# Kernel optimization log

Measured on AMD Instinct MI355X. Metric: run time of the kernel, lower is better.

The kernel has to match this reference:

```python
import jax, jax.numpy as jnp
import numpy as np

N_NODES = 50000
N_EDGES = 800000


def _gcn_conv(x, W, b, src, dst, norm, n_nodes):
    # PyG GCNConv: out = D^{-1/2} (A + I) D^{-1/2} (x W) + b
    h = x @ W                                  # [N, out]
    msg = h[src] * norm[:, None]               # [E+N, out] gathered, normalized messages
    agg = jax.ops.segment_sum(msg, dst, num_segments=n_nodes)
    return agg + b


def _build_norm(edge_index, n_nodes):
    # add self-loops, compute symmetric degree normalization
    loop = jnp.arange(n_nodes, dtype=edge_index.dtype)
    src = jnp.concatenate([edge_index[0], loop])
    dst = jnp.concatenate([edge_index[1], loop])
    deg = jnp.zeros((n_nodes,), jnp.float32).at[dst].add(1.0)
    dinv = jnp.where(deg > 0, jax.lax.rsqrt(deg), 0.0)
    norm = dinv[src] * dinv[dst]
    return src, dst, norm


def setup_inputs() -> dict:
    key = jax.random.key(0)
    ks = jax.random.split(key, 5)
    x = jax.random.normal(ks[0], (N_NODES, 128), dtype=jnp.float32)
    edge_index = jax.random.randint(ks[1], (2, N_EDGES), 0, N_NODES, dtype=jnp.int64)
    s1 = 1.0 / np.sqrt(128)
    s2 = 1.0 / np.sqrt(128)
    s3 = 1.0 / np.sqrt(64)
    return {
        "x": x,
        "edge_index": edge_index,
        "W1": jax.random.normal(ks[2], (128, 128), dtype=jnp.float32) * s1,
        "b1": jnp.zeros((128,), jnp.float32),
        "W2": jax.random.normal(ks[3], (128, 64), dtype=jnp.float32) * s2,
        "b2": jnp.zeros((64,), jnp.float32),
        "W3": jax.random.normal(ks[4], (64, 128), dtype=jnp.float32) * s3,
        "b3": jnp.zeros((128,), jnp.float32),
    }


def reference(x, edge_index, W1, b1, W2, b2, W3, b3):
    n = x.shape[0]
    src, dst, norm = _build_norm(edge_index, n)
    # dropout is identity in eval mode
    h = jax.nn.relu(_gcn_conv(x, W1, b1, src, dst, norm, n))
    h = jax.nn.relu(_gcn_conv(h, W2, b2, src, dst, norm, n))
    out = _gcn_conv(h, W3, b3, src, dst, norm, n)
    return out
```

## Files before the change

kernel.cpp:

```cpp
#include <hip/hip_runtime.h>


#define DEV_INLINE __device__ __forceinline__

typedef unsigned int uint;
typedef unsigned short ushort;
typedef __attribute__((ext_vector_type(8))) short bf16x8;
typedef __attribute__((ext_vector_type(4))) float f32x4;

static DEV_INLINE uint f2bf_rne(float f) {
    uint u = __float_as_uint(f);
    return (u + 0x7FFFu + ((u >> 16) & 1u)) >> 16;
}
static DEV_INLINE uint pack2(float a, float b) { return f2bf_rne(a) | (f2bf_rne(b) << 16); }
static DEV_INLINE float bflo(uint u) { return __uint_as_float(u << 16); }
static DEV_INLINE float bfhi(uint u) { return __uint_as_float(u & 0xFFFF0000u); }

static DEV_INLINE void fma8(float4& a, float4& b, float n, const uint4& v) {
    a.x = fmaf(n, bflo(v.x), a.x); a.y = fmaf(n, bfhi(v.x), a.y);
    a.z = fmaf(n, bflo(v.y), a.z); a.w = fmaf(n, bfhi(v.y), a.w);
    b.x = fmaf(n, bflo(v.z), b.x); b.y = fmaf(n, bfhi(v.z), b.y);
    b.z = fmaf(n, bflo(v.w), b.z); b.w = fmaf(n, bfhi(v.w), b.w);
}

static DEV_INLINE void split8(const float4& x0, const float4& x1, bf16x8& ah, bf16x8& al) {
    float xs[8] = {x0.x, x0.y, x0.z, x0.w, x1.x, x1.y, x1.z, x1.w};
#pragma unroll
    for (int j = 0; j < 8; ++j) {
        uint u = __float_as_uint(xs[j]);
        ah[j] = (short)(u >> 16);
        float r = xs[j] - __uint_as_float(u & 0xFFFF0000u);
        al[j] = (short)(__float_as_uint(r) >> 16);
    }
}


__global__ __launch_bounds__(256) void hist_coarse_kernel(
    const int* __restrict__ dst, int* __restrict__ cnt196, int E, int NBK)
{
    __shared__ int h[256];
    if ((int)threadIdx.x < NBK) h[threadIdx.x] = 0;
    __syncthreads();
    for (int i = blockIdx.x * blockDim.x + threadIdx.x; i < E; i += gridDim.x * blockDim.x)
        atomicAdd(&h[dst[i] >> 8], 1);
    __syncthreads();
    if ((int)threadIdx.x < NBK) {
        int v = h[threadIdx.x];
        if (v) atomicAdd(&cnt196[threadIdx.x], v);
    }
}

__global__ void scan_coarse_kernel(const int* __restrict__ cnt196, int* __restrict__ base196,
                                   int* __restrict__ cursor196, int* __restrict__ rowptr,
                                   int NBK, int N, int E)
{
    __shared__ int buf[256];
    const int tid = threadIdx.x;
    int v = (tid < NBK) ? cnt196[tid] : 0;
    buf[tid] = v;
    __syncthreads();
#pragma unroll
    for (int ofs = 1; ofs < 256; ofs <<= 1) {
        int t = (tid >= ofs) ? buf[tid - ofs] : 0;
        __syncthreads();
        buf[tid] += t;
        __syncthreads();
    }
    if (tid < NBK) {
        int b = buf[tid] - v;
        base196[tid] = b;
        cursor196[tid] = b;
    }
    if (tid == 0) rowptr[N] = E;
}

__global__ __launch_bounds__(256) void scatter_coarse_kernel(
    const int* __restrict__ src, const int* __restrict__ dst,
    int* __restrict__ cursor196, uint* __restrict__ pkg, int E, int NBK)
{
    __shared__ int histL[256];
    __shared__ int baseL[256];
    const int tid = threadIdx.x;
    const int c0  = blockIdx.x * 2048;
    if (tid < NBK) histL[tid] = 0;
    __syncthreads();

    uint mypk[8];
    int  myn = 0;
#pragma unroll
    for (int k = 0; k < 8; ++k) {
        int idx = c0 + k * 256 + tid;
        if (idx < E) {
            uint pk = ((uint)dst[idx] << 16) | (uint)(src[idx] & 0xFFFF);
            mypk[myn++] = pk;
            atomicAdd(&histL[pk >> 24], 1);
        }
    }
    __syncthreads();
    if (tid < NBK) {
        int h = histL[tid];
        baseL[tid] = (h > 0) ? atomicAdd(&cursor196[tid], h) : 0;
        histL[tid] = 0;
    }
    __syncthreads();
    for (int k = 0; k < myn; ++k) {
        uint pk = mypk[k];
        int b = pk >> 24;
        int pos = baseL[b] + atomicAdd(&histL[b], 1);
        pkg[pos] = pk;
    }
}

__global__ __launch_bounds__(256) void build_fine_kernel(
    const uint* __restrict__ pkg, const int* __restrict__ cnt196,
    const int* __restrict__ base196, int* __restrict__ rowptr,
    float* __restrict__ dinv, ushort* __restrict__ perm, int N)
{
    __shared__ uint   pkL[8192];
    __shared__ ushort outS[8192];
    __shared__ int hist[256];
    __shared__ int buf[256];
    const int b   = blockIdx.x;
    const int tid = threadIdx.x;
    const int base = base196[b];
    int nE = cnt196[b];
    if (nE > 8192) nE = 8192;

    hist[tid] = 0;
    __syncthreads();
    for (int i = tid; i < nE; i += 256) {
        uint pk = pkg[base + i];
        pkL[i] = pk;
        atomicAdd(&hist[(pk >> 16) & 255], 1);
    }
    __syncthreads();

    int cnt = hist[tid];
    buf[tid] = cnt;
    __syncthreads();
#pragma unroll
    for (int ofs = 1; ofs < 256; ofs <<= 1) {
        int t = (tid >= ofs) ? buf[tid - ofs] : 0;
        __syncthreads();
        buf[tid] += t;
        __syncthreads();
    }
    int excl = buf[tid] - cnt;
    int node = b * 256 + tid;
    if (node < N) {
        rowptr[node] = base + excl;
        dinv[node]   = rsqrtf((float)(cnt + 1));
    }
    hist[tid] = excl;
    __syncthreads();
    for (int i = tid; i < nE; i += 256) {
        uint pk = pkL[i];
        int d = (pk >> 16) & 255;
        int pos = atomicAdd(&hist[d], 1);
        outS[pos] = (ushort)(pk & 0xFFFFu);
    }
    __syncthreads();
    for (int i = tid; i < nE; i += 256) perm[base + i] = outS[i];
}


template<int K, int NOUT>
static DEV_INLINE void prep_one(const float* __restrict__ W,
                                ushort* __restrict__ Wh, ushort* __restrict__ Wl, int id) {
    constexpr int C = NOUT / 16;
    int lane = id & 63;
    int tc   = id >> 6;
    int c = tc % C, t = tc / C;
    int krow = t * 32 + (lane >> 4) * 8;
    int col  = c * 16 + (lane & 15);
#pragma unroll
    for (int j = 0; j < 8; ++j) {
        float w = W[(size_t)(krow + j) * NOUT + col];
        uint u = __float_as_uint(w);
        Wh[(size_t)id * 8 + j] = (ushort)(u >> 16);
        float r = w - __uint_as_float(u & 0xFFFF0000u);
        Wl[(size_t)id * 8 + j] = (ushort)(__float_as_uint(r) >> 16);
    }
}

__global__ void prep_wfrag_all_kernel(
    const float* __restrict__ W1, const float* __restrict__ W2, const float* __restrict__ W3,
    ushort* w1h, ushort* w1l, ushort* w2h, ushort* w2l, ushort* w3h, ushort* w3l)
{
    int id = blockIdx.x * 256 + threadIdx.x;
    if (id < 2048)       prep_one<128, 128>(W1, w1h, w1l, id);
    else if (id < 3072)  prep_one<128, 64>(W2, w2h, w2l, id - 2048);
    else if (id < 4096)  prep_one<64, 128>(W3, w3h, w3l, id - 3072);
}


template<int K, int NOUT, bool ABF, bool PRE, bool POSTB, bool OUTBF>
__global__ __launch_bounds__(256) void gemm_mfma_kernel(
    const void* __restrict__ A, const ushort* __restrict__ Whf, const ushort* __restrict__ Wlf,
    const float* __restrict__ bias_k, const float* __restrict__ bias_n,
    void* __restrict__ Cout, int N)
{
    constexpr int C  = NOUT / 16;
    constexpr int T  = K / 32;
    const int tid  = threadIdx.x;
    const int w    = tid >> 6;
    const int lane = tid & 63;
    const int row0 = blockIdx.x * 64 + w * 16;

    const int arow  = row0 + (lane & 15);
    const int arowc = (arow < N) ? arow : (N - 1);
    const int lq    = (lane >> 4);

    const bf16x8* WH = reinterpret_cast<const bf16x8*>(Whf);
    const bf16x8* WL = reinterpret_cast<const bf16x8*>(Wlf);

    f32x4 acc[C];
#pragma unroll
    for (int c = 0; c < C; ++c) acc[c] = (f32x4){0.f, 0.f, 0.f, 0.f};

#pragma unroll
    for (int t = 0; t < T; ++t) {
        bf16x8 ah, al;
        if (ABF) {
            const ushort* ap = (const ushort*)A + (size_t)arowc * K + t * 32 + lq * 8;
            ah = *reinterpret_cast<const bf16x8*>(ap);
        } else {
            const float* ap = (const float*)A + (size_t)arowc * K + t * 32 + lq * 8;
            float4 x0 = *reinterpret_cast<const float4*>(ap);
            float4 x1 = *reinterpret_cast<const float4*>(ap + 4);
            if (PRE) {
                const float* bp = bias_k + t * 32 + lq * 8;
                float4 b0 = *reinterpret_cast<const float4*>(bp);
                float4 b1 = *reinterpret_cast<const float4*>(bp + 4);
                x0.x = fmaxf(x0.x + b0.x, 0.f); x0.y = fmaxf(x0.y + b0.y, 0.f);
                x0.z = fmaxf(x0.z + b0.z, 0.f); x0.w = fmaxf(x0.w + b0.w, 0.f);
                x1.x = fmaxf(x1.x + b1.x, 0.f); x1.y = fmaxf(x1.y + b1.y, 0.f);
                x1.z = fmaxf(x1.z + b1.z, 0.f); x1.w = fmaxf(x1.w + b1.w, 0.f);
            }
            split8(x0, x1, ah, al);
        }
#pragma unroll
        for (int c = 0; c < C; ++c) {
            bf16x8 bh = WH[(t * C + c) * 64 + lane];
            bf16x8 bl = WL[(t * C + c) * 64 + lane];
            acc[c] = __builtin_amdgcn_mfma_f32_16x16x32_bf16(ah, bh, acc[c], 0, 0, 0);
            if (!ABF)
                acc[c] = __builtin_amdgcn_mfma_f32_16x16x32_bf16(al, bh, acc[c], 0, 0, 0);
            acc[c] = __builtin_amdgcn_mfma_f32_16x16x32_bf16(ah, bl, acc[c], 0, 0, 0);
        }
    }

    const int rbase = (lane >> 4) * 4;
    const int ccol  = (lane & 15);
#pragma unroll
    for (int c = 0; c < C; ++c) {
        int col = c * 16 + ccol;
        float pb = POSTB ? bias_n[col] : 0.f;
#pragma unroll
        for (int r = 0; r < 4; ++r) {
            int row = row0 + rbase + r;
            if (row < N) {
                float v = acc[c][r] + pb;
                if (OUTBF) ((ushort*)Cout)[(size_t)row * NOUT + col] = (ushort)f2bf_rne(v);
                else       ((float*)Cout)[(size_t)row * NOUT + col] = v;
            }
        }
    }
}


template<int F, bool BIAS, bool RELU, bool OUTBF>
__global__ __launch_bounds__(256) void agg_gather_kernel(
    const uint* __restrict__ H, const int* __restrict__ rowptr,
    const ushort* __restrict__ perm_src, const float* __restrict__ dinv,
    const float* __restrict__ bias, void* __restrict__ OUT, int N)
{
    constexpr int GROUP = F / 8;
    constexpr int FW    = F / 2;
    constexpr int NPB   = 256 / GROUP;
    const int lane = threadIdx.x % GROUP;
    const int g    = threadIdx.x / GROUP;
    const int node = blockIdx.x * NPB + g;
    if (node >= N) return;

    const int beg = rowptr[node];
    const int end = rowptr[node + 1];
    const float di = dinv[node];

    float4 aA = make_float4(0.f, 0.f, 0.f, 0.f), aB = aA;
    float4 bA = aA, bB = aA;
    {
        uint4 v = reinterpret_cast<const uint4*>(H + (size_t)node * FW)[lane];
        fma8(aA, aB, di * di, v);
    }

    int e = beg;
    for (; e + 3 < end; e += 4) {
        int s0 = perm_src[e];     int s1 = perm_src[e + 1];
        int s2 = perm_src[e + 2]; int s3 = perm_src[e + 3];
        float n0 = dinv[s0] * di, n1 = dinv[s1] * di;
        float n2 = dinv[s2] * di, n3 = dinv[s3] * di;
        uint4 v0 = reinterpret_cast<const uint4*>(H + (size_t)s0 * FW)[lane];
        uint4 v1 = reinterpret_cast<const uint4*>(H + (size_t)s1 * FW)[lane];
        uint4 v2 = reinterpret_cast<const uint4*>(H + (size_t)s2 * FW)[lane];
        uint4 v3 = reinterpret_cast<const uint4*>(H + (size_t)s3 * FW)[lane];
        fma8(aA, aB, n0, v0);
        fma8(bA, bB, n1, v1);
        fma8(aA, aB, n2, v2);
        fma8(bA, bB, n3, v3);
    }
    for (; e < end; ++e) {
        int s0 = perm_src[e];
        float n0 = dinv[s0] * di;
        uint4 v0 = reinterpret_cast<const uint4*>(H + (size_t)s0 * FW)[lane];
        fma8(aA, aB, n0, v0);
    }
    aA.x += bA.x; aA.y += bA.y; aA.z += bA.z; aA.w += bA.w;
    aB.x += bB.x; aB.y += bB.y; aB.z += bB.z; aB.w += bB.w;

    if (BIAS) {
        const float4* b4 = reinterpret_cast<const float4*>(bias);
        float4 c0 = b4[lane * 2], c1 = b4[lane * 2 + 1];
        aA.x += c0.x; aA.y += c0.y; aA.z += c0.z; aA.w += c0.w;
        aB.x += c1.x; aB.y += c1.y; aB.z += c1.z; aB.w += c1.w;
    }
    if (RELU) {
        aA.x = fmaxf(aA.x, 0.f); aA.y = fmaxf(aA.y, 0.f);
        aA.z = fmaxf(aA.z, 0.f); aA.w = fmaxf(aA.w, 0.f);
        aB.x = fmaxf(aB.x, 0.f); aB.y = fmaxf(aB.y, 0.f);
        aB.z = fmaxf(aB.z, 0.f); aB.w = fmaxf(aB.w, 0.f);
    }

    if (OUTBF) {
        uint4 u;
        u.x = pack2(aA.x, aA.y); u.y = pack2(aA.z, aA.w);
        u.z = pack2(aB.x, aB.y); u.w = pack2(aB.z, aB.w);
        reinterpret_cast<uint4*>((uint*)OUT + (size_t)node * FW)[lane] = u;
    } else {
        float4* O = reinterpret_cast<float4*>((float*)OUT + (size_t)node * F);
        O[lane * 2]     = aA;
        O[lane * 2 + 1] = aB;
    }
}


static inline size_t align_up(size_t v, size_t a) { return (v + a - 1) / a * a; }

extern "C" void kernel_launch(void* const* d_in, const int* in_sizes, int n_in,
                              void* d_out, int out_size, void* d_ws, size_t ws_size,
                              hipStream_t stream) {
    const float* x  = (const float*)d_in[0];
    const int*   ei = (const int*)d_in[1];
    const float* W1 = (const float*)d_in[2];
    const float* b1 = (const float*)d_in[3];
    const float* W2 = (const float*)d_in[4];
    const float* b2 = (const float*)d_in[5];
    const float* W3 = (const float*)d_in[6];
    const float* b3 = (const float*)d_in[7];
    float* out = (float*)d_out;

    const int N = in_sizes[0] / 128;
    const int E = in_sizes[1] / 2;
    const int* src = ei;
    const int* dst = ei + E;
    const int NBK = (N + 255) / 256;

    char* ws = (char*)d_ws;
    size_t off = 0;
    float* dinv   = (float*)(ws + off); off = align_up(off + (size_t)N * 4, 512);
    int*   rowptr = (int*)  (ws + off); off = align_up(off + (size_t)(N + 1) * 4, 512);
    int*   cnt196    = (int*)(ws + off); off = align_up(off + (size_t)NBK * 4, 512);
    int*   base196   = (int*)(ws + off); off = align_up(off + (size_t)NBK * 4, 512);
    int*   cursor196 = (int*)(ws + off); off = align_up(off + (size_t)NBK * 4, 512);
    ushort* perm_src = (ushort*)(ws + off); off = align_up(off + (size_t)E * 2, 512);
    uint*  pkg    = (uint*) (ws + off); off = align_up(off + (size_t)E * 4, 512);
    uint*  Hbf    = (uint*) (ws + off); off = align_up(off + (size_t)N * 128 * 2, 512);
    char*  Ashare = (char*) (ws + off); off = align_up(off + (size_t)N * 128 * 4, 512);
    ushort* w1h   = (ushort*)(ws + off); off = align_up(off + (size_t)128 * 128 * 2, 512);
    ushort* w1l   = (ushort*)(ws + off); off = align_up(off + (size_t)128 * 128 * 2, 512);
    ushort* w2h   = (ushort*)(ws + off); off = align_up(off + (size_t)128 * 64 * 2, 512);
    ushort* w2l   = (ushort*)(ws + off); off = align_up(off + (size_t)128 * 64 * 2, 512);
    ushort* w3h   = (ushort*)(ws + off); off = align_up(off + (size_t)64 * 128 * 2, 512);
    ushort* w3l   = (ushort*)(ws + off); off = align_up(off + (size_t)64 * 128 * 2, 512);
    (void)ws_size;

    uint* H1bf   = Hbf;
    uint* H2bf   = Hbf;
    uint* H3bf   = Hbf + (size_t)N * 32;
    uint* AGG1bf = (uint*)Ashare;
    float* T     = (float*)Ashare;

    const int TPB = 256;
    dim3 blk(TPB);
    int gRow = (N + 63) / 64;

    prep_wfrag_all_kernel<<<16, blk, 0, stream>>>(W1, W2, W3, w1h, w1l, w2h, w2l, w3h, w3l);

    hipMemsetAsync(cnt196, 0, (size_t)NBK * 4, stream);
    hist_coarse_kernel<<<392, blk, 0, stream>>>(dst, cnt196, E, NBK);
    scan_coarse_kernel<<<1, blk, 0, stream>>>(cnt196, base196, cursor196, rowptr, NBK, N, E);
    scatter_coarse_kernel<<<(E + 2047) / 2048, blk, 0, stream>>>(src, dst, cursor196, pkg, E, NBK);
    build_fine_kernel<<<NBK, blk, 0, stream>>>(pkg, cnt196, base196, rowptr, dinv, perm_src, N);

    gemm_mfma_kernel<128, 128, false, false, false, true><<<gRow, blk, 0, stream>>>(
        x, w1h, w1l, nullptr, nullptr, H1bf, N);
    agg_gather_kernel<128, true, true, true><<<(N + 15) / 16, blk, 0, stream>>>(
        H1bf, rowptr, perm_src, dinv, b1, AGG1bf, N);

    gemm_mfma_kernel<128, 64, true, false, false, true><<<gRow, blk, 0, stream>>>(
        AGG1bf, w2h, w2l, nullptr, nullptr, H2bf, N);
    agg_gather_kernel<64, true, true, true><<<(N + 31) / 32, blk, 0, stream>>>(
        H2bf, rowptr, perm_src, dinv, b2, H3bf, N);

    agg_gather_kernel<64, false, false, false><<<(N + 31) / 32, blk, 0, stream>>>(
        H3bf, rowptr, perm_src, dinv, nullptr, T, N);
    gemm_mfma_kernel<64, 128, false, false, true, false><<<gRow, blk, 0, stream>>>(
        T, w3h, w3l, nullptr, b3, out, N);
}
```

Measured before the change: 229.6 us.

## Fuse scatter with first GEMM and use finer 128-node CSR buckets

```diff
diff --git a/kernel.cpp b/kernel.cpp
--- a/kernel.cpp
+++ b/kernel.cpp
@@ -12,7 +12,6 @@
     uint u = __float_as_uint(f);
     return (u + 0x7FFFu + ((u >> 16) & 1u)) >> 16;
 }
-static DEV_INLINE uint pack2(float a, float b) { return f2bf_rne(a) | (f2bf_rne(b) << 16); }
 static DEV_INLINE float bflo(uint u) { return __uint_as_float(u << 16); }
 static DEV_INLINE float bfhi(uint u) { return __uint_as_float(u & 0xFFFF0000u); }
 
@@ -32,135 +31,6 @@
         float r = xs[j] - __uint_as_float(u & 0xFFFF0000u);
         al[j] = (short)(__float_as_uint(r) >> 16);
     }
-}
-
-
-__global__ __launch_bounds__(256) void hist_coarse_kernel(
-    const int* __restrict__ dst, int* __restrict__ cnt196, int E, int NBK)
-{
-    __shared__ int h[256];
-    if ((int)threadIdx.x < NBK) h[threadIdx.x] = 0;
-    __syncthreads();
-    for (int i = blockIdx.x * blockDim.x + threadIdx.x; i < E; i += gridDim.x * blockDim.x)
-        atomicAdd(&h[dst[i] >> 8], 1);
-    __syncthreads();
-    if ((int)threadIdx.x < NBK) {
-        int v = h[threadIdx.x];
-        if (v) atomicAdd(&cnt196[threadIdx.x], v);
-    }
-}
-
-__global__ void scan_coarse_kernel(const int* __restrict__ cnt196, int* __restrict__ base196,
-                                   int* __restrict__ cursor196, int* __restrict__ rowptr,
-                                   int NBK, int N, int E)
-{
-    __shared__ int buf[256];
-    const int tid = threadIdx.x;
-    int v = (tid < NBK) ? cnt196[tid] : 0;
-    buf[tid] = v;
-    __syncthreads();
-#pragma unroll
-    for (int ofs = 1; ofs < 256; ofs <<= 1) {
-        int t = (tid >= ofs) ? buf[tid - ofs] : 0;
-        __syncthreads();
-        buf[tid] += t;
-        __syncthreads();
-    }
-    if (tid < NBK) {
-        int b = buf[tid] - v;
-        base196[tid] = b;
-        cursor196[tid] = b;
-    }
-    if (tid == 0) rowptr[N] = E;
-}
-
-__global__ __launch_bounds__(256) void scatter_coarse_kernel(
-    const int* __restrict__ src, const int* __restrict__ dst,
-    int* __restrict__ cursor196, uint* __restrict__ pkg, int E, int NBK)
-{
-    __shared__ int histL[256];
-    __shared__ int baseL[256];
-    const int tid = threadIdx.x;
-    const int c0  = blockIdx.x * 2048;
-    if (tid < NBK) histL[tid] = 0;
-    __syncthreads();
-
-    uint mypk[8];
-    int  myn = 0;
-#pragma unroll
-    for (int k = 0; k < 8; ++k) {
-        int idx = c0 + k * 256 + tid;
-        if (idx < E) {
-            uint pk = ((uint)dst[idx] << 16) | (uint)(src[idx] & 0xFFFF);
-            mypk[myn++] = pk;
-            atomicAdd(&histL[pk >> 24], 1);
-        }
-    }
-    __syncthreads();
-    if (tid < NBK) {
-        int h = histL[tid];
-        baseL[tid] = (h > 0) ? atomicAdd(&cursor196[tid], h) : 0;
-        histL[tid] = 0;
-    }
-    __syncthreads();
-    for (int k = 0; k < myn; ++k) {
-        uint pk = mypk[k];
-        int b = pk >> 24;
-        int pos = baseL[b] + atomicAdd(&histL[b], 1);
-        pkg[pos] = pk;
-    }
-}
-
-__global__ __launch_bounds__(256) void build_fine_kernel(
-    const uint* __restrict__ pkg, const int* __restrict__ cnt196,
-    const int* __restrict__ base196, int* __restrict__ rowptr,
-    float* __restrict__ dinv, ushort* __restrict__ perm, int N)
-{
-    __shared__ uint   pkL[8192];
-    __shared__ ushort outS[8192];
-    __shared__ int hist[256];
-    __shared__ int buf[256];
-    const int b   = blockIdx.x;
-    const int tid = threadIdx.x;
-    const int base = base196[b];
-    int nE = cnt196[b];
-    if (nE > 8192) nE = 8192;
-
-    hist[tid] = 0;
-    __syncthreads();
-    for (int i = tid; i < nE; i += 256) {
-        uint pk = pkg[base + i];
-        pkL[i] = pk;
-        atomicAdd(&hist[(pk >> 16) & 255], 1);
-    }
-    __syncthreads();
-
-    int cnt = hist[tid];
-    buf[tid] = cnt;
-    __syncthreads();
-#pragma unroll
-    for (int ofs = 1; ofs < 256; ofs <<= 1) {
-        int t = (tid >= ofs) ? buf[tid - ofs] : 0;
-        __syncthreads();
-        buf[tid] += t;
-        __syncthreads();
-    }
-    int excl = buf[tid] - cnt;
-    int node = b * 256 + tid;
-    if (node < N) {
-        rowptr[node] = base + excl;
-        dinv[node]   = rsqrtf((float)(cnt + 1));
-    }
-    hist[tid] = excl;
-    __syncthreads();
-    for (int i = tid; i < nE; i += 256) {
-        uint pk = pkL[i];
-        int d = (pk >> 16) & 255;
-        int pos = atomicAdd(&hist[d], 1);
-        outS[pos] = (ushort)(pk & 0xFFFFu);
-    }
-    __syncthreads();
-    for (int i = tid; i < nE; i += 256) perm[base + i] = outS[i];
 }
 
 
@@ -183,29 +53,75 @@
     }
 }
 
-__global__ void prep_wfrag_all_kernel(
+__global__ __launch_bounds__(256) void prep_zero_kernel(
     const float* __restrict__ W1, const float* __restrict__ W2, const float* __restrict__ W3,
-    ushort* w1h, ushort* w1l, ushort* w2h, ushort* w2l, ushort* w3h, ushort* w3l)
-{
-    int id = blockIdx.x * 256 + threadIdx.x;
-    if (id < 2048)       prep_one<128, 128>(W1, w1h, w1l, id);
-    else if (id < 3072)  prep_one<128, 64>(W2, w2h, w2l, id - 2048);
-    else if (id < 4096)  prep_one<64, 128>(W3, w3h, w3l, id - 3072);
-}
-
-
-template<int K, int NOUT, bool ABF, bool PRE, bool POSTB, bool OUTBF>
-__global__ __launch_bounds__(256) void gemm_mfma_kernel(
-    const void* __restrict__ A, const ushort* __restrict__ Whf, const ushort* __restrict__ Wlf,
-    const float* __restrict__ bias_k, const float* __restrict__ bias_n,
-    void* __restrict__ Cout, int N)
+    ushort* w1h, ushort* w1l, ushort* w2h, ushort* w2l, ushort* w3h, ushort* w3l,
+    int* __restrict__ cnt, int NBK2)
+{
+    const int bid = blockIdx.x, tid = threadIdx.x;
+    if (bid < 16) {
+        int id = bid * 256 + tid;
+        if (id < 2048)       prep_one<128, 128>(W1, w1h, w1l, id);
+        else if (id < 3072)  prep_one<128, 64>(W2, w2h, w2l, id - 2048);
+        else if (id < 4096)  prep_one<64, 128>(W3, w3h, w3l, id - 3072);
+    } else {
+        for (int j = tid; j < NBK2; j += 256) cnt[j] = 0;
+    }
+}
+
+
+__global__ __launch_bounds__(256) void hist_kernel(
+    const int* __restrict__ dst, int* __restrict__ cnt, int E, int NBK2)
+{
+    __shared__ int h[512];
+    const int tid = threadIdx.x, bid = blockIdx.x, G = gridDim.x;
+    for (int j = tid; j < NBK2; j += 256) h[j] = 0;
+    __syncthreads();
+    for (int i = bid * 256 + tid; i < E; i += G * 256)
+        atomicAdd(&h[dst[i] >> 7], 1);
+    __syncthreads();
+    for (int j = tid; j < NBK2; j += 256) {
+        int v = h[j];
+        if (v) atomicAdd(&cnt[j], v);
+    }
+}
+
+__global__ __launch_bounds__(256) void scan_kernel(
+    const int* __restrict__ cnt, int* __restrict__ base, int* __restrict__ cursor,
+    int* __restrict__ rowptr, int NBK2, int N, int E)
+{
+    __shared__ int buf[512];
+    const int tid = threadIdx.x;
+    for (int j = tid; j < 512; j += 256) buf[j] = (j < NBK2) ? cnt[j] : 0;
+    __syncthreads();
+    for (int ofs = 1; ofs < 256; ofs <<= 1) {
+        int a = (tid >= ofs) ? buf[tid - ofs] : 0;
+        int b = (tid >= ofs) ? buf[256 + tid - ofs] : 0;
+        __syncthreads();
+        buf[tid] += a; buf[256 + tid] += b;
+        __syncthreads();
+    }
+    int tot0 = buf[255];
+    for (int j = tid; j < NBK2; j += 256) {
+        int incl = buf[j] + ((j >= 256) ? tot0 : 0);
+        int ex = incl - cnt[j];
+        base[j] = ex; cursor[j] = ex;
+    }
+    if (tid == 0) rowptr[N] = E;
+}
+
+
+template<int K, int NOUT, bool ABF, bool POSTB, bool OUTBF>
+static DEV_INLINE void gemm_body(const void* __restrict__ A,
+                                 const ushort* __restrict__ Whf, const ushort* __restrict__ Wlf,
+                                 const float* __restrict__ bias_n,
+                                 void* __restrict__ Cout, int N, int vt, int tid)
 {
     constexpr int C  = NOUT / 16;
     constexpr int T  = K / 32;
-    const int tid  = threadIdx.x;
     const int w    = tid >> 6;
     const int lane = tid & 63;
-    const int row0 = blockIdx.x * 64 + w * 16;
+    const int row0 = vt * 64 + w * 16;
 
     const int arow  = row0 + (lane & 15);
     const int arowc = (arow < N) ? arow : (N - 1);
@@ -228,15 +144,6 @@
             const float* ap = (const float*)A + (size_t)arowc * K + t * 32 + lq * 8;
             float4 x0 = *reinterpret_cast<const float4*>(ap);
             float4 x1 = *reinterpret_cast<const float4*>(ap + 4);
-            if (PRE) {
-                const float* bp = bias_k + t * 32 + lq * 8;
-                float4 b0 = *reinterpret_cast<const float4*>(bp);
-                float4 b1 = *reinterpret_cast<const float4*>(bp + 4);
-                x0.x = fmaxf(x0.x + b0.x, 0.f); x0.y = fmaxf(x0.y + b0.y, 0.f);
-                x0.z = fmaxf(x0.z + b0.z, 0.f); x0.w = fmaxf(x0.w + b0.w, 0.f);
-                x1.x = fmaxf(x1.x + b1.x, 0.f); x1.y = fmaxf(x1.y + b1.y, 0.f);
-                x1.z = fmaxf(x1.z + b1.z, 0.f); x1.w = fmaxf(x1.w + b1.w, 0.f);
-            }
             split8(x0, x1, ah, al);
         }
 #pragma unroll
@@ -253,19 +160,120 @@
     const int rbase = (lane >> 4) * 4;
     const int ccol  = (lane & 15);
 #pragma unroll
-    for (int c = 0; c < C; ++c) {
-        int col = c * 16 + ccol;
-        float pb = POSTB ? bias_n[col] : 0.f;
-#pragma unroll
-        for (int r = 0; r < 4; ++r) {
-            int row = row0 + rbase + r;
-            if (row < N) {
-                float v = acc[c][r] + pb;
+    for (int r = 0; r < 4; ++r) {
+        int row = row0 + rbase + r;
+        if (row < N) {
+#pragma unroll
+            for (int c = 0; c < C; ++c) {
+                int col = c * 16 + ccol;
+                float v = acc[c][r];
+                if (POSTB) v += bias_n[col];
                 if (OUTBF) ((ushort*)Cout)[(size_t)row * NOUT + col] = (ushort)f2bf_rne(v);
                 else       ((float*)Cout)[(size_t)row * NOUT + col] = v;
             }
         }
     }
+}
+
+__global__ __launch_bounds__(256) void scatter_gemm1_kernel(
+    const int* __restrict__ src, const int* __restrict__ dst,
+    int* __restrict__ cursor, uint* __restrict__ pkg, int E, int NBK2, int nchunks,
+    const float* __restrict__ x, const ushort* __restrict__ w1h,
+    const ushort* __restrict__ w1l, ushort* __restrict__ H1, int N)
+{
+    __shared__ int S[1024];
+    const int bid = blockIdx.x, tid = threadIdx.x;
+    if (bid < nchunks) {
+        int* histL = S;
+        int* baseL = S + 512;
+        const int c0 = bid * 2048;
+        for (int j = tid; j < NBK2; j += 256) histL[j] = 0;
+        __syncthreads();
+#pragma unroll
+        for (int k = 0; k < 8; ++k) {
+            int idx = c0 + k * 256 + tid;
+            if (idx < E) atomicAdd(&histL[dst[idx] >> 7], 1);
+        }
+        __syncthreads();
+        for (int j = tid; j < NBK2; j += 256) {
+            int h = histL[j];
+            baseL[j] = h ? atomicAdd(&cursor[j], h) : 0;
+            histL[j] = 0;
+        }
+        __syncthreads();
+#pragma unroll
+        for (int k = 0; k < 8; ++k) {
+            int idx = c0 + k * 256 + tid;
+            if (idx < E) {
+                int d = dst[idx];
+                int b = d >> 7;
+                int pos = baseL[b] + atomicAdd(&histL[b], 1);
+                pkg[pos] = ((uint)d << 16) | (uint)(src[idx] & 0xFFFF);
+            }
+        }
+    } else {
+        gemm_body<128, 128, false, false, true>(x, w1h, w1l, nullptr, H1, N,
+                                                bid - nchunks, tid);
+    }
+}
+
+__global__ __launch_bounds__(256) void build_kernel(
+    const uint* __restrict__ pkg, const int* __restrict__ cnt,
+    const int* __restrict__ base392, int* __restrict__ rowptr,
+    float* __restrict__ dinv, ushort* __restrict__ perm, int N)
+{
+    __shared__ uint S[6400];
+    uint*   pkL  = S;
+    ushort* outS = (ushort*)(S + 4096);
+    int*    hist = (int*)(S + 6144);
+    int*    buf  = (int*)(S + 6272);
+    const int vb = blockIdx.x, tid = threadIdx.x;
+    const int base = base392[vb];
+    int nE = cnt[vb]; if (nE > 4096) nE = 4096;
+
+    if (tid < 128) hist[tid] = 0;
+    __syncthreads();
+    for (int i = tid; i < nE; i += 256) {
+        uint pk = pkg[base + i];
+        pkL[i] = pk;
+        atomicAdd(&hist[(pk >> 16) & 127], 1);
+    }
+    __syncthreads();
+    if (tid < 128) buf[tid] = hist[tid];
+    __syncthreads();
+    for (int ofs = 1; ofs < 128; ofs <<= 1) {
+        int t = (tid < 128 && tid >= ofs) ? buf[tid - ofs] : 0;
+        __syncthreads();
+        if (tid < 128) buf[tid] += t;
+        __syncthreads();
+    }
+    if (tid < 128) {
+        int c = hist[tid];
+        int ex = buf[tid] - c;
+        int node = vb * 128 + tid;
+        if (node < N) {
+            rowptr[node] = base + ex;
+            dinv[node]   = rsqrtf((float)(c + 1));
+        }
+        hist[tid] = ex;
+    }
+    __syncthreads();
+    for (int i = tid; i < nE; i += 256) {
+        uint pk = pkL[i];
+        int pos = atomicAdd(&hist[(pk >> 16) & 127], 1);
+        outS[pos] = (ushort)(pk & 0xFFFFu);
+    }
+    __syncthreads();
+    for (int i = tid; i < nE; i += 256) perm[base + i] = outS[i];
+}
+
+
+template<int K, int NOUT, bool ABF, bool POSTB, bool OUTBF>
+__global__ __launch_bounds__(256) void gemm_kernel(
+    const void* __restrict__ A, const ushort* __restrict__ Wh, const ushort* __restrict__ Wl,
+    const float* __restrict__ bn, void* __restrict__ C, int N)
+{
+    gemm_body<K, NOUT, ABF, POSTB, OUTBF>(A, Wh, Wl, bn, C, N, blockIdx.x, threadIdx.x);
 }
 
 
@@ -333,8 +341,10 @@
 
     if (OUTBF) {
         uint4 u;
-        u.x = pack2(aA.x, aA.y); u.y = pack2(aA.z, aA.w);
-        u.z = pack2(aB.x, aB.y); u.w = pack2(aB.z, aB.w);
+        u.x = f2bf_rne(aA.x) | (f2bf_rne(aA.y) << 16);
+        u.y = f2bf_rne(aA.z) | (f2bf_rne(aA.w) << 16);
+        u.z = f2bf_rne(aB.x) | (f2bf_rne(aB.y) << 16);
+        u.w = f2bf_rne(aB.z) | (f2bf_rne(aB.w) << 16);
         reinterpret_cast<uint4*>((uint*)OUT + (size_t)node * FW)[lane] = u;
     } else {
         float4* O = reinterpret_cast<float4*>((float*)OUT + (size_t)node * F);
@@ -363,57 +373,52 @@
     const int E = in_sizes[1] / 2;
     const int* src = ei;
     const int* dst = ei + E;
-    const int NBK = (N + 255) / 256;
+    const int NBK2    = (N + 127) / 128;
+    const int nchunks = (E + 2047) / 2048;
+    const int gRow    = (N + 63) / 64;
 
     char* ws = (char*)d_ws;
     size_t off = 0;
-    float* dinv   = (float*)(ws + off); off = align_up(off + (size_t)N * 4, 512);
-    int*   rowptr = (int*)  (ws + off); off = align_up(off + (size_t)(N + 1) * 4, 512);
-    int*   cnt196    = (int*)(ws + off); off = align_up(off + (size_t)NBK * 4, 512);
-    int*   base196   = (int*)(ws + off); off = align_up(off + (size_t)NBK * 4, 512);
-    int*   cursor196 = (int*)(ws + off); off = align_up(off + (size_t)NBK * 4, 512);
-    ushort* perm_src = (ushort*)(ws + off); off = align_up(off + (size_t)E * 2, 512);
-    uint*  pkg    = (uint*) (ws + off); off = align_up(off + (size_t)E * 4, 512);
-    uint*  Hbf    = (uint*) (ws + off); off = align_up(off + (size_t)N * 128 * 2, 512);
-    char*  Ashare = (char*) (ws + off); off = align_up(off + (size_t)N * 128 * 4, 512);
-    ushort* w1h   = (ushort*)(ws + off); off = align_up(off + (size_t)128 * 128 * 2, 512);
-    ushort* w1l   = (ushort*)(ws + off); off = align_up(off + (size_t)128 * 128 * 2, 512);
-    ushort* w2h   = (ushort*)(ws + off); off = align_up(off + (size_t)128 * 64 * 2, 512);
-    ushort* w2l   = (ushort*)(ws + off); off = align_up(off + (size_t)128 * 64 * 2, 512);
-    ushort* w3h   = (ushort*)(ws + off); off = align_up(off + (size_t)64 * 128 * 2, 512);
-    ushort* w3l   = (ushort*)(ws + off); off = align_up(off + (size_t)64 * 128 * 2, 512);
+    float* dinv    = (float*)(ws + off); off = align_up(off + (size_t)N * 4, 512);
+    int*   rowptr  = (int*)  (ws + off); off = align_up(off + (size_t)(N + 1) * 4, 512);
+    int*   cnt     = (int*)  (ws + off); off = align_up(off + (size_t)NBK2 * 4, 512);
+    int*   base392 = (int*)  (ws + off); off = align_up(off + (size_t)NBK2 * 4, 512);
+    int*   cursor  = (int*)  (ws + off); off = align_up(off + (size_t)NBK2 * 4, 512);
+    ushort* perm   = (ushort*)(ws + off); off = align_up(off + (size_t)E * 2, 512);
+    uint*  pkg     = (uint*) (ws + off); off = align_up(off + (size_t)E * 4, 512);
+    uint*  regA    = (uint*) (ws + off); off = align_up(off + (size_t)N * 64 * 4, 512);
+    uint*  regB    = (uint*) (ws + off); off = align_up(off + (size_t)N * 64 * 4, 512);
+    ushort* w1h = (ushort*)(ws + off); off = align_up(off + (size_t)128 * 128 * 2, 512);
+    ushort* w1l = (ushort*)(ws + off); off = align_up(off + (size_t)128 * 128 * 2, 512);
+    ushort* w2h = (ushort*)(ws + off); off = align_up(off + (size_t)128 * 64 * 2, 512);
+    ushort* w2l = (ushort*)(ws + off); off = align_up(off + (size_t)128 * 64 * 2, 512);
+    ushort* w3h = (ushort*)(ws + off); off = align_up(off + (size_t)64 * 128 * 2, 512);
+    ushort* w3l = (ushort*)(ws + off); off = align_up(off + (size_t)64 * 128 * 2, 512);
     (void)ws_size;
 
-    uint* H1bf   = Hbf;
-    uint* H2bf   = Hbf;
-    uint* H3bf   = Hbf + (size_t)N * 32;
-    uint* AGG1bf = (uint*)Ashare;
-    float* T     = (float*)Ashare;
-
-    const int TPB = 256;
-    dim3 blk(TPB);
-    int gRow = (N + 63) / 64;
-
-    prep_wfrag_all_kernel<<<16, blk, 0, stream>>>(W1, W2, W3, w1h, w1l, w2h, w2l, w3h, w3l);
-
-    hipMemsetAsync(cnt196, 0, (size_t)NBK * 4, stream);
-    hist_coarse_kernel<<<392, blk, 0, stream>>>(dst, cnt196, E, NBK);
-    scan_coarse_kernel<<<1, blk, 0, stream>>>(cnt196, base196, cursor196, rowptr, NBK, N, E);
-    scatter_coarse_kernel<<<(E + 2047) / 2048, blk, 0, stream>>>(src, dst, cursor196, pkg, E, NBK);
-    build_fine_kernel<<<NBK, blk, 0, stream>>>(pkg, cnt196, base196, rowptr, dinv, perm_src, N);
-
-    gemm_mfma_kernel<128, 128, false, false, false, true><<<gRow, blk, 0, stream>>>(
-        x, w1h, w1l, nullptr, nullptr, H1bf, N);
+    uint*  H1bf = regA;
+    uint*  AGG1 = regB;
+    uint*  H2bf = regA;
+    uint*  H3bf = regA + (size_t)N * 32;
+    float* T    = (float*)regB;
+
+    dim3 blk(256);
+
+    prep_zero_kernel<<<17, blk, 0, stream>>>(W1, W2, W3, w1h, w1l, w2h, w2l, w3h, w3l,
+                                             cnt, NBK2);
+    hist_kernel<<<392, blk, 0, stream>>>(dst, cnt, E, NBK2);
+    scan_kernel<<<1, blk, 0, stream>>>(cnt, base392, cursor, rowptr, NBK2, N, E);
+    scatter_gemm1_kernel<<<nchunks + gRow, blk, 0, stream>>>(
+        src, dst, cursor, pkg, E, NBK2, nchunks, x, w1h, w1l, (ushort*)H1bf, N);
+    build_kernel<<<NBK2, blk, 0, stream>>>(pkg, cnt, base392, rowptr, dinv, perm, N);
     agg_gather_kernel<128, true, true, true><<<(N + 15) / 16, blk, 0, stream>>>(
-        H1bf, rowptr, perm_src, dinv, b1, AGG1bf, N);
-
-    gemm_mfma_kernel<128, 64, true, false, false, true><<<gRow, blk, 0, stream>>>(
-        AGG1bf, w2h, w2l, nullptr, nullptr, H2bf, N);
+        H1bf, rowptr, perm, dinv, b1, AGG1, N);
+    gemm_kernel<128, 64, true, false, true><<<gRow, blk, 0, stream>>>(
+        AGG1, w2h, w2l, nullptr, H2bf, N);
     agg_gather_kernel<64, true, true, true><<<(N + 31) / 32, blk, 0, stream>>>(
-        H2bf, rowptr, perm_src, dinv, b2, H3bf, N);
-
+        H2bf, rowptr, perm, dinv, b2, H3bf, N);
     agg_gather_kernel<64, false, false, false><<<(N + 31) / 32, blk, 0, stream>>>(
-        H3bf, rowptr, perm_src, dinv, nullptr, T, N);
-    gemm_mfma_kernel<64, 128, false, false, true, false><<<gRow, blk, 0, stream>>>(
-        T, w3h, w3l, nullptr, b3, out, N);
-}
+        H3bf, rowptr, perm, dinv, nullptr, T, N);
+    gemm_kernel<64, 128, false, true, false><<<gRow, blk, 0, stream>>>(
+        T, w3h, w3l, b3, out, N);
+}
```

Result: faster. 220.4 us (-4.0%).
